# Kernel optimization log

Measured on AMD Instinct MI355X. Metric: run time of the kernel, lower is better.

## Reference

```python
import jax, jax.numpy as jnp
import numpy as np

C_IN = 512
C_QK = C_IN // 8
B, H, W = 8, 96, 96


def setup_inputs() -> dict:
    key = jax.random.key(0)
    ks = jax.random.split(key, 8)
    s = 1.0 / np.sqrt(C_IN)
    return {
        "x": jax.random.normal(ks[0], (B, C_IN, H, W), dtype=jnp.float32),
        "Wq": jax.random.normal(ks[1], (C_QK, C_IN), dtype=jnp.float32) * s,
        "bq": jnp.zeros((C_QK,), dtype=jnp.float32),
        "Wk": jax.random.normal(ks[2], (C_QK, C_IN), dtype=jnp.float32) * s,
        "bk": jnp.zeros((C_QK,), dtype=jnp.float32),
        "Wv": jax.random.normal(ks[3], (C_IN, C_IN), dtype=jnp.float32) * s,
        "bv": jnp.zeros((C_IN,), dtype=jnp.float32),
        "gamma": jnp.zeros((1,), dtype=jnp.float32),
    }


def reference(x, Wq, bq, Wk, bk, Wv, bv, gamma):
    Bb, Cc, Hh, Ww = x.shape
    # 1x1 convs as channel GEMMs
    q = jnp.einsum('bchw,oc->bohw', x, Wq) + bq[None, :, None, None]
    k = jnp.einsum('bchw,oc->bohw', x, Wk) + bk[None, :, None, None]
    v = jnp.einsum('bchw,oc->bohw', x, Wv) + bv[None, :, None, None]
    # vertical (column) energy: query at (h,w) vs keys at (g,w); diag h==g masked to -inf
    eH = jnp.einsum('bchw,bcgw->bhwg', q, k)  # [B,H,W,H]
    diag = jnp.eye(Hh, dtype=bool)[:, None, :]  # [H,1,H] broadcasts over w
    eH = jnp.where(diag[None], -jnp.inf, eH)
    # horizontal (row) energy: query at (h,w) vs keys at (h,u)
    eW = jnp.einsum('bchw,bchu->bhwu', q, k)  # [B,H,W,W]
    # joint softmax over concatenated H+W axis
    att = jax.nn.softmax(jnp.concatenate([eH, eW], axis=-1), axis=-1)
    aH, aW = att[..., :Hh], att[..., Hh:]
    out_H = jnp.einsum('bhwg,bcgw->bchw', aH, v)
    out_W = jnp.einsum('bhwu,bchu->bchw', aW, v)
    return gamma * (out_H + out_W) + x
```

## Files before the change

### kernel.cpp

```cpp
#include <hip/hip_runtime.h>
#include <math.h>

constexpr int nB = 8;
constexpr int nC = 512;
constexpr int nH = 96;
constexpr int nW = 96;
constexpr int nP = nH * nW;
constexpr int nCQK = 64;
constexpr int nS = nH + nW;
constexpr int nO = 640;
constexpr int nM = nB * nP;

using short8  = __attribute__((ext_vector_type(8))) short;
using ushort8 = __attribute__((ext_vector_type(8))) unsigned short;
using floatx4 = __attribute__((ext_vector_type(4))) float;

__device__ inline unsigned pack_bf16(float a, float b) {
    unsigned ua = __float_as_uint(a), ub = __float_as_uint(b);
    ua = (ua + 0x7fff + ((ua >> 16) & 1)) >> 16;
    ub = (ub + 0x7fff + ((ub >> 16) & 1)) >> 16;
    return ua | (ub << 16);
}
__device__ inline ushort f2bf(float a) {
    unsigned ua = __float_as_uint(a);
    return (ushort)((ua + 0x7fff + ((ua >> 16) & 1)) >> 16);
}
__device__ inline float bf2f(ushort u) {
    return __uint_as_float((unsigned)u << 16);
}

__global__ __launch_bounds__(256) void transpose_kernel(
    const float* __restrict__ x, ushort* __restrict__ xT)
{
    __shared__ float T[64 * 65];
    const int b = blockIdx.z, p0 = blockIdx.x * 64, c0 = blockIdx.y * 64;
    const int tid = threadIdx.x;
    #pragma unroll
    for (int it = 0; it < 4; ++it) {
        int c  = it * 16 + (tid >> 4);
        int p4 = (tid & 15) * 4;
        float4 v = *(const float4*)&x[((size_t)b * nC + c0 + c) * nP + p0 + p4];
        T[c * 65 + p4 + 0] = v.x; T[c * 65 + p4 + 1] = v.y;
        T[c * 65 + p4 + 2] = v.z; T[c * 65 + p4 + 3] = v.w;
    }
    __syncthreads();
    #pragma unroll
    for (int it = 0; it < 8; ++it) {
        int idx = it * 256 + tid;
        int p = idx >> 5;
        int c = (idx & 31) * 2;
        unsigned u = pack_bf16(T[c * 65 + p], T[(c + 1) * 65 + p]);
        *(unsigned*)&xT[((size_t)b * nP + p0 + p) * nC + c0 + c] = u;
    }
}

__global__ __launch_bounds__(256) void wconv_kernel(
    const float* __restrict__ Wq, const float* __restrict__ bq,
    const float* __restrict__ Wk, const float* __restrict__ bk,
    const float* __restrict__ Wv, const float* __restrict__ bv,
    ushort* __restrict__ Wc, float* __restrict__ bc)
{
    const int o = blockIdx.x, t = threadIdx.x;
    const float *src, *bsrc; int oo;
    if (o < 64)       { src = Wq; bsrc = bq; oo = o; }
    else if (o < 128) { src = Wk; bsrc = bk; oo = o - 64; }
    else              { src = Wv; bsrc = bv; oo = o - 128; }
    float2 v = *(const float2*)&src[(size_t)oo * nC + t * 2];
    *(unsigned*)&Wc[(size_t)o * nC + t * 2] = pack_bf16(v.x, v.y);
    if (t == 0) bc[o] = bsrc[oo];
}

__global__ __launch_bounds__(256) void mfma_proj_kernel(
    const ushort* __restrict__ xT, const ushort* __restrict__ Wc,
    const float* __restrict__ bc, float* __restrict__ qk,
    ushort* __restrict__ vW)
{
    __shared__ ushort As[128 * 40];
    __shared__ ushort Bs[128 * 40];
    const int tid = threadIdx.x;
    const int m0 = blockIdx.x * 128;
    const int o0 = blockIdx.y * 128;

    const int sm  = tid >> 2;
    const int skp = tid & 3;
    const ushort* pa0 = xT + (size_t)(m0 + sm) * nC + skp * 8;
    const ushort* pa1 = xT + (size_t)(m0 + sm + 64) * nC + skp * 8;
    const ushort* pb0 = Wc + (size_t)(o0 + sm) * nC + skp * 8;
    const ushort* pb1 = Wc + (size_t)(o0 + sm + 64) * nC + skp * 8;
    ushort* la0 = &As[sm * 40 + skp * 8];
    ushort* la1 = &As[(sm + 64) * 40 + skp * 8];
    ushort* lb0 = &Bs[sm * 40 + skp * 8];
    ushort* lb1 = &Bs[(sm + 64) * 40 + skp * 8];

    const int lane = tid & 63;
    const int wave = tid >> 6;
    const int wr = wave & 1, wc = wave >> 1;
    const int lm = lane & 15, q = lane >> 4;
    int aoff[4], boff[4];
    #pragma unroll
    for (int i = 0; i < 4; ++i) aoff[i] = (wr * 64 + i * 16 + lm) * 40 + q * 8;
    #pragma unroll
    for (int j = 0; j < 4; ++j) boff[j] = (wc * 64 + j * 16 + lm) * 40 + q * 8;

    floatx4 acc[4][4];
    #pragma unroll
    for (int i = 0; i < 4; ++i)
        #pragma unroll
        for (int j = 0; j < 4; ++j) acc[i][j] = (floatx4){0.f, 0.f, 0.f, 0.f};

    const bool vmode = (o0 != 0);

    for (int k0 = 0; k0 < nC; k0 += 32) {
        uint4 a0 = *(const uint4*)(pa0 + k0);
        uint4 a1 = *(const uint4*)(pa1 + k0);
        uint4 b0 = *(const uint4*)(pb0 + k0);
        uint4 b1 = *(const uint4*)(pb1 + k0);
        if (k0) __syncthreads();
        *(uint4*)la0 = a0; *(uint4*)la1 = a1;
        *(uint4*)lb0 = b0; *(uint4*)lb1 = b1;
        __syncthreads();
        short8 av[4], bvv[4];
        #pragma unroll
        for (int i = 0; i < 4; ++i) av[i] = *(const short8*)&As[aoff[i]];
        #pragma unroll
        for (int j = 0; j < 4; ++j) bvv[j] = *(const short8*)&Bs[boff[j]];
        if (!vmode) {
            #pragma unroll
            for (int i = 0; i < 4; ++i)
                #pragma unroll
                for (int j = 0; j < 4; ++j)
                    acc[i][j] = __builtin_amdgcn_mfma_f32_16x16x32_bf16(
                        av[i], bvv[j], acc[i][j], 0, 0, 0);
        } else {
            #pragma unroll
            for (int i = 0; i < 4; ++i)
                #pragma unroll
                for (int j = 0; j < 4; ++j)
                    acc[i][j] = __builtin_amdgcn_mfma_f32_16x16x32_bf16(
                        bvv[i], av[j], acc[i][j], 0, 0, 0);
        }
    }

    if (!vmode) {
        float bj[4];
        #pragma unroll
        for (int j = 0; j < 4; ++j) bj[j] = bc[wc * 64 + j * 16 + lm];
        #pragma unroll
        for (int i = 0; i < 4; ++i) {
            #pragma unroll
            for (int r = 0; r < 4; ++r) {
                int mrow = m0 + wr * 64 + i * 16 + q * 4 + r;
                float* orow = qk + (size_t)mrow * 128 + wc * 64 + lm;
                #pragma unroll
                for (int j = 0; j < 4; ++j) orow[j * 16] = acc[i][j][r] + bj[j];
            }
        }
    } else {
        const int b  = m0 / nP;
        const int p0 = m0 - b * nP;
        #pragma unroll
        for (int i = 0; i < 4; ++i) {
            #pragma unroll
            for (int r = 0; r < 4; ++r) {
                int o = o0 + wc * 64 + i * 16 + q * 4 + r;
                float bias = bc[o];
                int c = o - 128;
                ushort* vrow = vW + ((size_t)(b * nC + c)) * nP + p0 + wr * 64 + lm;
                #pragma unroll
                for (int j = 0; j < 4; ++j)
                    vrow[j * 16] = f2bf(acc[i][j][r] + bias);
            }
        }
    }
}

__global__ __launch_bounds__(256) void vtrans_kernel(
    const ushort* __restrict__ vW, ushort* __restrict__ vH)
{
    __shared__ ushort T[96 * 128];
    const int c = blockIdx.x, b = blockIdx.y, tid = threadIdx.x;
    const size_t base = ((size_t)(b * nC + c)) * nP;
    for (int l = tid; l < 96 * 12; l += 256) {
        int hh = l / 12, seg = l % 12;
        uint4 u = *(const uint4*)&vW[base + (size_t)hh * nW + seg * 8];
        *(uint4*)&T[hh * 128 + ((seg ^ ((hh >> 3) & 7)) * 8)] = u;
    }
    __syncthreads();
    for (int l = tid; l < 96 * 12; l += 256) {
        int ww = l / 12, seg = l % 12;
        ushort8 vv;
        #pragma unroll
        for (int e = 0; e < 8; ++e) {
            int hh = seg * 8 + e;
            int phys = (((ww >> 3) ^ ((hh >> 3) & 7)) * 8) + (ww & 7);
            vv[e] = T[hh * 128 + phys];
        }
        *(ushort8*)&vH[base + (size_t)ww * nH + seg * 8] = vv;
    }
}

__global__ __launch_bounds__(256) void score_kernel(
    const float* __restrict__ qk, float* __restrict__ att, int mode)
{
    __shared__ float Qs[96][68];
    __shared__ float Ks[96][68];
    const int b   = blockIdx.y;
    const int fix = blockIdx.x;
    const int tid = threadIdx.x;

    for (int l = tid; l < 96 * 16; l += 256) {
        int r  = l / 16;
        int c4 = (l % 16) * 4;
        size_t p = (mode == 0) ? ((size_t)r * nW + fix) : ((size_t)fix * nW + r);
        const float* row = &qk[((size_t)b * nP + p) * 128];
        *(float4*)&Qs[r][c4] = *(const float4*)&row[c4];
        *(float4*)&Ks[r][c4] = *(const float4*)&row[64 + c4];
    }
    __syncthreads();

    const int tx = tid % 16;
    const int ty = tid / 16;
    float acc[6][6] = {};
    for (int c4 = 0; c4 < nCQK; c4 += 4) {
        float4 qv[6], kv[6];
        #pragma unroll
        for (int i = 0; i < 6; ++i) qv[i] = *(const float4*)&Qs[ty + 16 * i][c4];
        #pragma unroll
        for (int j = 0; j < 6; ++j) kv[j] = *(const float4*)&Ks[tx + 16 * j][c4];
        #pragma unroll
        for (int i = 0; i < 6; ++i)
            #pragma unroll
            for (int j = 0; j < 6; ++j)
                acc[i][j] += qv[i].x * kv[j].x + qv[i].y * kv[j].y
                           + qv[i].z * kv[j].z + qv[i].w * kv[j].w;
    }

    #pragma unroll
    for (int i = 0; i < 6; ++i) {
        int row = ty + 16 * i;
        #pragma unroll
        for (int j = 0; j < 6; ++j) {
            int col = tx + 16 * j;
            float val = acc[i][j];
            if (mode == 0) {
                if (col == row) val = -INFINITY;
                att[((size_t)b * nP + row * nW + fix) * nS + col] = val;
            } else {
                att[((size_t)b * nP + fix * nW + row) * nS + 96 + col] = val;
            }
        }
    }
}

__global__ __launch_bounds__(256) void softmax_kernel(
    const float* __restrict__ att, ushort* __restrict__ attb)
{
    const int wav  = threadIdx.x / 64;
    const int lane = threadIdx.x % 64;
    const size_t pix = (size_t)blockIdx.x * 4 + wav;
    const float* a = att + pix * nS;
    ushort* ab = attb + pix * nS;
    float v0 = a[lane], v1 = a[lane + 64], v2 = a[lane + 128];
    float m = fmaxf(fmaxf(v0, v1), v2);
    #pragma unroll
    for (int off = 32; off; off >>= 1) m = fmaxf(m, __shfl_xor(m, off));
    float e0 = __expf(v0 - m), e1 = __expf(v1 - m), e2 = __expf(v2 - m);
    float s = e0 + e1 + e2;
    #pragma unroll
    for (int off = 32; off; off >>= 1) s += __shfl_xor(s, off);
    float inv = 1.0f / s;
    ab[lane]       = f2bf(e0 * inv);
    ab[lane + 64]  = f2bf(e1 * inv);
    ab[lane + 128] = f2bf(e2 * inv);
}

__global__ __launch_bounds__(256) void aggH_kernel(
    const ushort* __restrict__ attb, const ushort* __restrict__ vH,
    ushort* __restrict__ oh)
{
    __shared__ ushort As[96 * 104];
    __shared__ ushort Bs[128 * 104];
    const int b = blockIdx.y, w = blockIdx.x, tid = threadIdx.x;

    for (int l = tid; l < 96 * 12; l += 256) {
        int h = l / 12, seg = l % 12;
        uint4 u = *(const uint4*)&attb[((size_t)(b * nP + h * nW + w)) * nS + seg * 8];
        *(uint4*)&As[h * 104 + seg * 8] = u;
    }
    const int lane = tid & 63, wave = tid >> 6;
    const int wr = wave & 1, wc = wave >> 1;
    const int lm = lane & 15, q = lane >> 4;
    int aoff[3], boff[4];
    #pragma unroll
    for (int i = 0; i < 3; ++i) aoff[i] = (wr * 48 + i * 16 + lm) * 104 + q * 8;
    #pragma unroll
    for (int j = 0; j < 4; ++j) boff[j] = (wc * 64 + j * 16 + lm) * 104 + q * 8;

    for (int ct = 0; ct < 4; ++ct) {
        if (ct) __syncthreads();
        for (int l = tid; l < 128 * 12; l += 256) {
            int cl = l / 12, seg = l % 12;
            uint4 u = *(const uint4*)&vH[((size_t)(b * nC + ct * 128 + cl)) * nP
                                         + w * nH + seg * 8];
            *(uint4*)&Bs[cl * 104 + seg * 8] = u;
        }
        __syncthreads();
        floatx4 acc[3][4];
        #pragma unroll
        for (int i = 0; i < 3; ++i)
            #pragma unroll
            for (int j = 0; j < 4; ++j) acc[i][j] = (floatx4){0.f, 0.f, 0.f, 0.f};
        #pragma unroll
        for (int ks = 0; ks < 3; ++ks) {
            short8 av[3], bvv[4];
            #pragma unroll
            for (int i = 0; i < 3; ++i) av[i] = *(const short8*)&As[aoff[i] + ks * 32];
            #pragma unroll
            for (int j = 0; j < 4; ++j) bvv[j] = *(const short8*)&Bs[boff[j] + ks * 32];
            #pragma unroll
            for (int i = 0; i < 3; ++i)
                #pragma unroll
                for (int j = 0; j < 4; ++j)
                    acc[i][j] = __builtin_amdgcn_mfma_f32_16x16x32_bf16(
                        av[i], bvv[j], acc[i][j], 0, 0, 0);
        }
        #pragma unroll
        for (int i = 0; i < 3; ++i) {
            #pragma unroll
            for (int r = 0; r < 4; ++r) {
                int h = wr * 48 + i * 16 + q * 4 + r;
                ushort* orow = oh + ((size_t)(b * nP + h * nW + w)) * nC
                               + ct * 128 + wc * 64 + lm;
                #pragma unroll
                for (int j = 0; j < 4; ++j) orow[j * 16] = f2bf(acc[i][j][r]);
            }
        }
    }
}

__global__ __launch_bounds__(256) void aggW_kernel(
    const ushort* __restrict__ attb, const ushort* __restrict__ vW,
    const ushort* __restrict__ oh, const float* __restrict__ x,
    const float* __restrict__ gamma, float* __restrict__ out)
{
    __shared__ ushort As[96 * 104];
    __shared__ ushort Bs[64 * 104];
    __shared__ ushort Os[96 * 72];
    const int b = blockIdx.y, h = blockIdx.x, tid = threadIdx.x;
    const float gm = gamma[0];

    for (int l = tid; l < 96 * 12; l += 256) {
        int ww = l / 12, seg = l % 12;
        uint4 u = *(const uint4*)&attb[((size_t)(b * nP + h * nW + ww)) * nS
                                       + 96 + seg * 8];
        *(uint4*)&As[ww * 104 + seg * 8] = u;
    }
    const int lane = tid & 63, wave = tid >> 6;
    const int wr = wave & 1, wc = wave >> 1;
    const int lm = lane & 15, q = lane >> 4;
    int coff[2], woff[3];
    #pragma unroll
    for (int i = 0; i < 2; ++i) coff[i] = (wc * 32 + i * 16 + lm) * 104 + q * 8;
    #pragma unroll
    for (int j = 0; j < 3; ++j) woff[j] = (wr * 48 + j * 16 + lm) * 104 + q * 8;

    for (int ct = 0; ct < 8; ++ct) {
        if (ct) __syncthreads();
        for (int l = tid; l < 64 * 12; l += 256) {
            int cl = l / 12, seg = l % 12;
            uint4 u = *(const uint4*)&vW[((size_t)(b * nC + ct * 64 + cl)) * nP
                                         + h * nW + seg * 8];
            *(uint4*)&Bs[cl * 104 + seg * 8] = u;
        }
        for (int l = tid; l < 96 * 8; l += 256) {
            int ww = l / 8, seg = l % 8;
            uint4 u = *(const uint4*)&oh[((size_t)(b * nP + h * nW + ww)) * nC
                                         + ct * 64 + seg * 8];
            *(uint4*)&Os[ww * 72 + seg * 8] = u;
        }
        __syncthreads();
        floatx4 acc[2][3];
        #pragma unroll
        for (int i = 0; i < 2; ++i)
            #pragma unroll
            for (int j = 0; j < 3; ++j) acc[i][j] = (floatx4){0.f, 0.f, 0.f, 0.f};
        #pragma unroll
        for (int ks = 0; ks < 3; ++ks) {
            short8 cv[2], wv[3];
            #pragma unroll
            for (int i = 0; i < 2; ++i) cv[i] = *(const short8*)&Bs[coff[i] + ks * 32];
            #pragma unroll
            for (int j = 0; j < 3; ++j) wv[j] = *(const short8*)&As[woff[j] + ks * 32];
            #pragma unroll
            for (int i = 0; i < 2; ++i)
                #pragma unroll
                for (int j = 0; j < 3; ++j)
                    acc[i][j] = __builtin_amdgcn_mfma_f32_16x16x32_bf16(
                        cv[i], wv[j], acc[i][j], 0, 0, 0);
        }
        #pragma unroll
        for (int i = 0; i < 2; ++i) {
            #pragma unroll
            for (int r = 0; r < 4; ++r) {
                int cl = wc * 32 + i * 16 + q * 4 + r;
                int c  = ct * 64 + cl;
                #pragma unroll
                for (int j = 0; j < 3; ++j) {
                    int ww = wr * 48 + j * 16 + lm;
                    size_t oidx = ((size_t)(b * nC + c) * nH + h) * nW + ww;
                    float ohv = bf2f(Os[ww * 72 + cl]);
                    out[oidx] = gm * (acc[i][j][r] + ohv) + x[oidx];
                }
            }
        }
    }
}

extern "C" void kernel_launch(void* const* d_in, const int* in_sizes, int n_in,
                              void* d_out, int out_size, void* d_ws, size_t ws_size,
                              hipStream_t stream)
{
    const float* x     = (const float*)d_in[0];
    const float* Wq    = (const float*)d_in[1];
    const float* bq    = (const float*)d_in[2];
    const float* Wk    = (const float*)d_in[3];
    const float* bk    = (const float*)d_in[4];
    const float* Wv    = (const float*)d_in[5];
    const float* bv    = (const float*)d_in[6];
    const float* gamma = (const float*)d_in[7];
    float* out = (float*)d_out;

    char* p = (char*)d_ws;
    ushort* xT  = (ushort*)p;
    ushort* vH  = (ushort*)p;
    p += (size_t)nM * nC * 2;
    float* qk   = (float*)p;
    p += (size_t)nM * 128 * 4;
    ushort* vW  = (ushort*)p;
    p += (size_t)nM * nC * 2;
    float* att  = (float*)p;
    ushort* Wc  = (ushort*)p;
    float* bc   = (float*)(p + (size_t)nO * nC * 2);
    p += (size_t)nM * nS * 4;
    ushort* attb = (ushort*)p;
    p += (size_t)nM * nS * 2;
    ushort* oh  = (ushort*)p;

    dim3 blk(256);
    transpose_kernel<<<dim3(nP / 64, nC / 64, nB), blk, 0, stream>>>(x, xT);
    wconv_kernel<<<dim3(nO), blk, 0, stream>>>(Wq, bq, Wk, bk, Wv, bv, Wc, bc);
    mfma_proj_kernel<<<dim3(nM / 128, nO / 128), blk, 0, stream>>>(xT, Wc, bc, qk, vW);
    vtrans_kernel<<<dim3(nC, nB), blk, 0, stream>>>(vW, vH);
    score_kernel<<<dim3(nW, nB), blk, 0, stream>>>(qk, att, 0);
    score_kernel<<<dim3(nH, nB), blk, 0, stream>>>(qk, att, 1);
    softmax_kernel<<<dim3(nB * nP / 4), blk, 0, stream>>>(att, attb);
    aggH_kernel<<<dim3(nW, nB), blk, 0, stream>>>(attb, vH, oh);
    aggW_kernel<<<dim3(nH, nB), blk, 0, stream>>>(attb, vW, oh, x, gamma, out);
}
```

Baseline: 581.2 us.

## Use direct global-to-LDS loads and XCD-aware block remapping in projection GEMM

The projection GEMM now stages A and B tiles with global_load_lds, writing straight into LDS instead of going through registers. LDS rows lose their padding and go from 40 to 32 elements. The grid becomes 1D, with a swizzle that spreads consecutive block IDs across the 8 XCDs so each one works on a contiguous chunk of tiles and reuses L2 better. The risks are LDS bank conflicts from the unpadded layout when fragments are read, and that the loop is still single-buffered, so load latency is not hidden.

```diff
diff --git a/kernel.cpp b/kernel.cpp
--- a/kernel.cpp
+++ b/kernel.cpp
@@ -29,6 +29,12 @@
     return __uint_as_float((unsigned)u << 16);
 }
 
+typedef __attribute__((address_space(3))) unsigned int lds_u32;
+typedef __attribute__((address_space(1))) const unsigned int glb_u32;
+__device__ inline void gl_lds16(const void* g, void* l) {
+    __builtin_amdgcn_global_load_lds((glb_u32*)g, (lds_u32*)l, 16, 0, 0);
+}
+
 __global__ __launch_bounds__(256) void transpose_kernel(
     const float* __restrict__ x, ushort* __restrict__ xT)
 {
@@ -75,32 +81,36 @@
     const float* __restrict__ bc, float* __restrict__ qk,
     ushort* __restrict__ vW)
 {
-    __shared__ ushort As[128 * 40];
-    __shared__ ushort Bs[128 * 40];
+    __shared__ ushort As[128 * 32];
+    __shared__ ushort Bs[128 * 32];
     const int tid = threadIdx.x;
-    const int m0 = blockIdx.x * 128;
-    const int o0 = blockIdx.y * 128;
-
-    const int sm  = tid >> 2;
-    const int skp = tid & 3;
-    const ushort* pa0 = xT + (size_t)(m0 + sm) * nC + skp * 8;
-    const ushort* pa1 = xT + (size_t)(m0 + sm + 64) * nC + skp * 8;
-    const ushort* pb0 = Wc + (size_t)(o0 + sm) * nC + skp * 8;
-    const ushort* pb1 = Wc + (size_t)(o0 + sm + 64) * nC + skp * 8;
-    ushort* la0 = &As[sm * 40 + skp * 8];
-    ushort* la1 = &As[(sm + 64) * 40 + skp * 8];
-    ushort* lb0 = &Bs[sm * 40 + skp * 8];
-    ushort* lb1 = &Bs[(sm + 64) * 40 + skp * 8];
+
+    constexpr int NWG   = (nM / 128) * (nO / 128);
+    constexpr int CHUNK = NWG / 8;
+    const int bid = blockIdx.x;
+    const int wg  = (bid & 7) * CHUNK + (bid >> 3);
+    const int mtile = wg / 5, ntile = wg % 5;
+    const int m0 = mtile * 128, o0 = ntile * 128;
 
     const int lane = tid & 63;
     const int wave = tid >> 6;
-    const int wr = wave & 1, wc = wave >> 1;
+
+    const ushort* gA0 = xT + (size_t)(m0 + wave * 16 + (lane >> 2)) * nC + (lane & 3) * 8;
+    const ushort* gA1 = gA0 + (size_t)64 * nC;
+    const ushort* gB0 = Wc + (size_t)(o0 + wave * 16 + (lane >> 2)) * nC + (lane & 3) * 8;
+    const ushort* gB1 = gB0 + (size_t)64 * nC;
+    ushort* lA0 = &As[wave * 16 * 32];
+    ushort* lA1 = &As[(wave * 16 + 64) * 32];
+    ushort* lB0 = &Bs[wave * 16 * 32];
+    ushort* lB1 = &Bs[(wave * 16 + 64) * 32];
+
+    const int wr = wave & 1, wcl = wave >> 1;
     const int lm = lane & 15, q = lane >> 4;
     int aoff[4], boff[4];
     #pragma unroll
-    for (int i = 0; i < 4; ++i) aoff[i] = (wr * 64 + i * 16 + lm) * 40 + q * 8;
-    #pragma unroll
-    for (int j = 0; j < 4; ++j) boff[j] = (wc * 64 + j * 16 + lm) * 40 + q * 8;
+    for (int i = 0; i < 4; ++i) aoff[i] = (wr * 64 + i * 16 + lm) * 32 + q * 8;
+    #pragma unroll
+    for (int j = 0; j < 4; ++j) boff[j] = (wcl * 64 + j * 16 + lm) * 32 + q * 8;
 
     floatx4 acc[4][4];
     #pragma unroll
@@ -108,16 +118,14 @@
         #pragma unroll
         for (int j = 0; j < 4; ++j) acc[i][j] = (floatx4){0.f, 0.f, 0.f, 0.f};
 
-    const bool vmode = (o0 != 0);
+    const bool vmode = (ntile != 0);
 
     for (int k0 = 0; k0 < nC; k0 += 32) {
-        uint4 a0 = *(const uint4*)(pa0 + k0);
-        uint4 a1 = *(const uint4*)(pa1 + k0);
-        uint4 b0 = *(const uint4*)(pb0 + k0);
-        uint4 b1 = *(const uint4*)(pb1 + k0);
         if (k0) __syncthreads();
-        *(uint4*)la0 = a0; *(uint4*)la1 = a1;
-        *(uint4*)lb0 = b0; *(uint4*)lb1 = b1;
+        gl_lds16(gA0 + k0, lA0);
+        gl_lds16(gA1 + k0, lA1);
+        gl_lds16(gB0 + k0, lB0);
+        gl_lds16(gB1 + k0, lB1);
         __syncthreads();
         short8 av[4], bvv[4];
         #pragma unroll
@@ -144,13 +152,13 @@
     if (!vmode) {
         float bj[4];
         #pragma unroll
-        for (int j = 0; j < 4; ++j) bj[j] = bc[wc * 64 + j * 16 + lm];
+        for (int j = 0; j < 4; ++j) bj[j] = bc[wcl * 64 + j * 16 + lm];
         #pragma unroll
         for (int i = 0; i < 4; ++i) {
             #pragma unroll
             for (int r = 0; r < 4; ++r) {
                 int mrow = m0 + wr * 64 + i * 16 + q * 4 + r;
-                float* orow = qk + (size_t)mrow * 128 + wc * 64 + lm;
+                float* orow = qk + (size_t)mrow * 128 + wcl * 64 + lm;
                 #pragma unroll
                 for (int j = 0; j < 4; ++j) orow[j * 16] = acc[i][j][r] + bj[j];
             }
@@ -162,7 +170,7 @@
         for (int i = 0; i < 4; ++i) {
             #pragma unroll
             for (int r = 0; r < 4; ++r) {
-                int o = o0 + wc * 64 + i * 16 + q * 4 + r;
+                int o = o0 + wcl * 64 + i * 16 + q * 4 + r;
                 float bias = bc[o];
                 int c = o - 128;
                 ushort* vrow = vW + ((size_t)(b * nC + c)) * nP + p0 + wr * 64 + lm;
@@ -449,7 +457,7 @@
     dim3 blk(256);
     transpose_kernel<<<dim3(nP / 64, nC / 64, nB), blk, 0, stream>>>(x, xT);
     wconv_kernel<<<dim3(nO), blk, 0, stream>>>(Wq, bq, Wk, bk, Wv, bv, Wc, bc);
-    mfma_proj_kernel<<<dim3(nM / 128, nO / 128), blk, 0, stream>>>(xT, Wc, bc, qk, vW);
+    mfma_proj_kernel<<<dim3((nM / 128) * (nO / 128)), blk, 0, stream>>>(xT, Wc, bc, qk, vW);
     vtrans_kernel<<<dim3(nC, nB), blk, 0, stream>>>(vW, vH);
     score_kernel<<<dim3(nW, nB), blk, 0, stream>>>(qk, att, 0);
     score_kernel<<<dim3(nH, nB), blk, 0, stream>>>(qk, att, 1);
```

Measured after the change: 586.9 us. About the same (+1.0%).
